# Kernel tuning notes

Hardware: AMD Instinct MI355X
Metric: run time of the kernel (lower is better)

Reference implementation:

```python
import jax, jax.numpy as jnp
import numpy as np

NUM_EXPERTS = 32
TOP_K = 4
HIDDEN = 2048
INTER = 768
N_TOKENS = 2048
NORM_TOPK = True


def setup_inputs() -> dict:
    key = jax.random.key(0)
    k0, k1, k2, k3 = jax.random.split(key, 4)
    hidden_states = jax.random.normal(k0, (N_TOKENS, HIDDEN), dtype=jnp.float32)
    # router gate: Linear(hidden, num_experts), stored as (h, E)
    Wg = jax.random.normal(k1, (HIDDEN, NUM_EXPERTS), dtype=jnp.float32) * 0.02
    # per-expert merged gate_up: (E, h, 2*i); down: (E, i, h)
    Wgu = jax.random.normal(k2, (NUM_EXPERTS, HIDDEN, 2 * INTER), dtype=jnp.float32) * 0.02
    Wd = jax.random.normal(k3, (NUM_EXPERTS, INTER, HIDDEN), dtype=jnp.float32) * 0.02
    return {"hidden_states": hidden_states, "Wg": Wg, "Wgu": Wgu, "Wd": Wd}


def reference(hidden_states, Wg, Wgu, Wd):
    E = Wgu.shape[0]
    # ---- routing ----
    router_logits = hidden_states @ Wg                       # (N, E)
    probs = jax.nn.softmax(router_logits.astype(jnp.float32), axis=-1)
    topk_w, topk_idx = jax.lax.top_k(probs, TOP_K)           # (N, K)
    if NORM_TOPK:
        topk_w = topk_w / jnp.sum(topk_w, axis=-1, keepdims=True)
    topk_w = topk_w.astype(hidden_states.dtype)
    # dense combine weights: (N, E), zero where expert not selected
    combine = jnp.einsum("nke,nk->ne", jax.nn.one_hot(topk_idx, E, dtype=topk_w.dtype), topk_w)
    # ---- experts (dense dispatch, zero-weighted combine == gather/scatter math) ----
    gate_up = jnp.einsum("nh,ehf->nef", hidden_states, Wgu)  # (N, E, 2i)
    gate, up = jnp.split(gate_up, 2, axis=-1)                # (N, E, i) each
    y = jax.nn.silu(gate) * up                               # SiluAndMul
    y = y * combine[:, :, None]                              # apply routing weight before down-proj (linear -> equivalent)
    out = jnp.einsum("nef,efh->nh", y, Wd)                   # (N, h)
    return out
```

## Files before the change

kernel.cpp:

```cpp
#include <hip/hip_runtime.h>
#include <hip/hip_bf16.h>

#define NE 32
#define TOPK 4
#define HID 2048
#define INTER 768
#define NT 2048
#define MAXTILE 64

typedef float f32x4 __attribute__((ext_vector_type(4)));
typedef float f32x2 __attribute__((ext_vector_type(2)));
typedef unsigned int u32x4 __attribute__((ext_vector_type(4)));
typedef unsigned int u32x2 __attribute__((ext_vector_type(2)));
typedef short short8 __attribute__((ext_vector_type(8)));
typedef __bf16 bf16x8 __attribute__((ext_vector_type(8)));

__device__ inline unsigned short f2bf(float f) {
  unsigned u = __builtin_bit_cast(unsigned, f);
  u += 0x7fffu + ((u >> 16) & 1u);
  return (unsigned short)(u >> 16);
}
__device__ inline unsigned pack2(unsigned short a, unsigned short b) {
  return (unsigned)a | ((unsigned)b << 16);
}
__device__ inline f32x4 mfma_bf16(short8 a, short8 b, f32x4 c) {
  return __builtin_amdgcn_mfma_f32_16x16x32_bf16(
      __builtin_bit_cast(bf16x8, a), __builtin_bit_cast(bf16x8, b), c, 0, 0, 0);
}
__device__ inline void gload16(const void* g, void* l) {
  __builtin_amdgcn_global_load_lds(
      (const __attribute__((address_space(1))) void*)g,
      (__attribute__((address_space(3))) void*)l, 16, 0, 0);
}

__global__ __launch_bounds__(64) void k_router(const float* __restrict__ X,
                                               const float* __restrict__ Wg,
                                               int* __restrict__ expert_of,
                                               float* __restrict__ weight_of,
                                               int* __restrict__ counts) {
  const int n = blockIdx.x;
  const int lane = threadIdx.x;
  const float* x = X + (size_t)n * HID;
  float acc[NE];
#pragma unroll
  for (int e = 0; e < NE; ++e) acc[e] = 0.f;
  for (int h = lane; h < HID; h += 64) {
    const float xv = x[h];
    const f32x4* wr = (const f32x4*)(Wg + (size_t)h * NE);
#pragma unroll
    for (int q = 0; q < NE / 4; ++q) {
      f32x4 w4 = wr[q];
      acc[q * 4 + 0] += xv * w4[0];
      acc[q * 4 + 1] += xv * w4[1];
      acc[q * 4 + 2] += xv * w4[2];
      acc[q * 4 + 3] += xv * w4[3];
    }
  }
#pragma unroll
  for (int off = 32; off >= 1; off >>= 1) {
#pragma unroll
    for (int e = 0; e < NE; ++e) acc[e] += __shfl_xor(acc[e], off, 64);
  }
  if (lane == 0) {
    float m = acc[0];
#pragma unroll
    for (int e = 1; e < NE; ++e) m = fmaxf(m, acc[e]);
    unsigned used = 0;
    int idx[TOPK];
    float wv[TOPK];
    float wsum = 0.f;
    for (int k = 0; k < TOPK; ++k) {
      int best = 0;
      float bv = -1e30f;
      for (int e = 0; e < NE; ++e) {
        if (!((used >> e) & 1u) && acc[e] > bv) { bv = acc[e]; best = e; }
      }
      used |= 1u << best;
      float w = expf(bv - m);
      idx[k] = best;
      wv[k] = w;
      wsum += w;
    }
    const float inv = 1.f / wsum;
    for (int k = 0; k < TOPK; ++k) {
      expert_of[n * TOPK + k] = idx[k];
      weight_of[n * TOPK + k] = wv[k] * inv;
      atomicAdd(&counts[idx[k]], 1);
    }
  }
}

__global__ void k_scan(const int* __restrict__ counts, int* __restrict__ offsets,
                       int* __restrict__ wl_e, int* __restrict__ wl_m,
                       int* __restrict__ wl_n) {
  int s = 0, t = 0;
  for (int e = 0; e < NE; ++e) {
    offsets[e] = s;
    const int c = counts[e];
    for (int m0 = 0; m0 < c; m0 += 256) {
      wl_e[t] = e;
      wl_m[t] = m0;
      ++t;
    }
    s += c;
  }
  offsets[NE] = s;
  *wl_n = t;
}

__global__ __launch_bounds__(64) void k_scatter(const int* __restrict__ expert_of,
                                                const float* __restrict__ weight_of,
                                                const int* __restrict__ offsets,
                                                int* __restrict__ slot_token,
                                                float* __restrict__ slot_w) {
  const int e = blockIdx.x;
  const int lane = threadIdx.x;
  int cnt = offsets[e];
  for (int a0 = 0; a0 < NT * TOPK; a0 += 64) {
    const int a = a0 + lane;
    const bool m = (expert_of[a] == e);
    const unsigned long long bal = __ballot(m);
    if (m) {
      const int pos = cnt + __popcll(bal & ((1ull << lane) - 1ull));
      slot_token[pos] = a >> 2;
      slot_w[pos] = weight_of[a];
    }
    cnt += __popcll(bal);
  }
}

__global__ __launch_bounds__(256) void k_xconv(const float* __restrict__ X,
                                               unsigned short* __restrict__ Xb) {
  const int i = blockIdx.x * 256 + threadIdx.x;
  const f32x4 v = ((const f32x4*)X)[i];
  u32x2 t = {pack2(f2bf(v[0]), f2bf(v[1])), pack2(f2bf(v[2]), f2bf(v[3]))};
  ((u32x2*)Xb)[i] = t;
}

__global__ __launch_bounds__(512) void k_gemm1(const unsigned short* __restrict__ Xb,
                                               const float* __restrict__ Wgu,
                                               const int* __restrict__ slot_token,
                                               const float* __restrict__ slot_w,
                                               const int* __restrict__ offsets,
                                               const int* __restrict__ wl_e,
                                               const int* __restrict__ wl_m,
                                               const int* __restrict__ wl_n,
                                               unsigned short* __restrict__ Y) {
  const int tile = blockIdx.x;
  if (tile >= *wl_n) return;
  const int e = wl_e[tile];
  const int m0 = wl_m[tile];
  const int base = offsets[e];
  const int ne = offsets[e + 1] - base;
  const int n0 = blockIdx.y * 64;
  const int tid = threadIdx.x;
  const int lane = tid & 63, w = tid >> 6;
  const int wm = w >> 1, wn = w & 1;
  const int fr = lane & 15, fo = lane >> 4;
  const int lr = lane >> 3, lk = lane & 7;

  __shared__ __attribute__((aligned(16))) unsigned short As[256 * 64];
  __shared__ __attribute__((aligned(16))) unsigned short Bg[64 * 64];
  __shared__ __attribute__((aligned(16))) unsigned short Bu[64 * 64];

  f32x4 accg[4][2], accu[4][2];
#pragma unroll
  for (int i = 0; i < 4; ++i)
#pragma unroll
    for (int j = 0; j < 2; ++j) {
      f32x4 z = {0.f, 0.f, 0.f, 0.f};
      accg[i][j] = z;
      accu[i][j] = z;
    }

  const unsigned short* asrc[4];
#pragma unroll
  for (int i = 0; i < 4; ++i) {
    const int ra = (w * 4 + i) * 8 + lr;
    const int tok = slot_token[base + min(m0 + ra, ne - 1)];
    asrc[i] = Xb + (size_t)tok * HID + ((lk ^ (ra & 7)) << 3);
  }

  const int np = tid & 31, kg = (tid >> 5) & 7, rg = tid >> 8;
  const float* bsrc = Wgu + (size_t)e * HID * (2 * INTER) + (size_t)(kg * 8) * (2 * INTER) +
                      rg * INTER + n0 + 2 * np;
  unsigned short* Bd = rg ? Bu : Bg;
  const int n_a = 2 * np, n_b = 2 * np + 1;
  const int wofa = n_a * 64 + ((kg ^ (n_a & 7)) << 3);
  const int wofb = n_b * 64 + ((kg ^ (n_b & 7)) << 3);

  for (int k0 = 0; k0 < HID; k0 += 64) {
#pragma unroll
    for (int i = 0; i < 4; ++i) gload16(asrc[i] + k0, &As[(w * 4 + i) * 512]);
    const float* bp = bsrc + (size_t)k0 * (2 * INTER);
    f32x2 bv[8];
#pragma unroll
    for (int j = 0; j < 8; ++j) bv[j] = *(const f32x2*)(bp + (size_t)j * (2 * INTER));
    u32x4 ta = {pack2(f2bf(bv[0][0]), f2bf(bv[1][0])), pack2(f2bf(bv[2][0]), f2bf(bv[3][0])),
                pack2(f2bf(bv[4][0]), f2bf(bv[5][0])), pack2(f2bf(bv[6][0]), f2bf(bv[7][0]))};
    u32x4 tb = {pack2(f2bf(bv[0][1]), f2bf(bv[1][1])), pack2(f2bf(bv[2][1]), f2bf(bv[3][1])),
                pack2(f2bf(bv[4][1]), f2bf(bv[5][1])), pack2(f2bf(bv[6][1]), f2bf(bv[7][1]))};
    *(u32x4*)&Bd[wofa] = ta;
    *(u32x4*)&Bd[wofb] = tb;
    __syncthreads();
#pragma unroll
    for (int ks = 0; ks < 2; ++ks) {
      const int c = ks * 4 + fo;
      short8 a[4], bg[2], bu[2];
#pragma unroll
      for (int mi = 0; mi < 4; ++mi) {
        const int row = wm * 64 + mi * 16 + fr;
        a[mi] = *(const short8*)&As[row * 64 + ((c ^ (row & 7)) << 3)];
      }
#pragma unroll
      for (int ni = 0; ni < 2; ++ni) {
        const int row = wn * 32 + ni * 16 + fr;
        const int off = row * 64 + ((c ^ (row & 7)) << 3);
        bg[ni] = *(const short8*)&Bg[off];
        bu[ni] = *(const short8*)&Bu[off];
      }
#pragma unroll
      for (int mi = 0; mi < 4; ++mi)
#pragma unroll
        for (int ni = 0; ni < 2; ++ni) {
          accg[mi][ni] = mfma_bf16(a[mi], bg[ni], accg[mi][ni]);
          accu[mi][ni] = mfma_bf16(a[mi], bu[ni], accu[mi][ni]);
        }
    }
    __syncthreads();
  }

#pragma unroll
  for (int mi = 0; mi < 4; ++mi) {
#pragma unroll
    for (int j = 0; j < 4; ++j) {
      const int gm = m0 + wm * 64 + mi * 16 + fo * 4 + j;
      if (gm < ne) {
        const float wgt = slot_w[base + gm];
        unsigned short* yp = Y + (size_t)(base + gm) * INTER + n0 + wn * 32;
#pragma unroll
        for (int ni = 0; ni < 2; ++ni) {
          const float g = accg[mi][ni][j];
          const float u = accu[mi][ni][j];
          const float yv = (g / (1.0f + __expf(-g))) * u * wgt;
          yp[ni * 16 + fr] = f2bf(yv);
        }
      }
    }
  }
}

__global__ __launch_bounds__(512) void k_gemm2(const unsigned short* __restrict__ Y,
                                               const float* __restrict__ Wd,
                                               const int* __restrict__ slot_token,
                                               const int* __restrict__ offsets,
                                               const int* __restrict__ wl_e,
                                               const int* __restrict__ wl_m,
                                               const int* __restrict__ wl_n,
                                               float* __restrict__ out) {
  const int tile = blockIdx.x;
  if (tile >= *wl_n) return;
  const int e = wl_e[tile];
  const int m0 = wl_m[tile];
  const int base = offsets[e];
  const int ne = offsets[e + 1] - base;
  const int n0 = blockIdx.y * 128;
  const int tid = threadIdx.x;
  const int lane = tid & 63, w = tid >> 6;
  const int wm = w >> 1, wn = w & 1;
  const int fr = lane & 15, fo = lane >> 4;
  const int lr = lane >> 3, lk = lane & 7;

  __shared__ __attribute__((aligned(16))) unsigned short As[256 * 64];
  __shared__ __attribute__((aligned(16))) unsigned short Bs[128 * 64];

  f32x4 acc[4][4];
#pragma unroll
  for (int i = 0; i < 4; ++i)
#pragma unroll
    for (int j = 0; j < 4; ++j) {
      f32x4 z = {0.f, 0.f, 0.f, 0.f};
      acc[i][j] = z;
    }

  const unsigned short* asrc[4];
#pragma unroll
  for (int i = 0; i < 4; ++i) {
    const int ra = (w * 4 + i) * 8 + lr;
    const int grow = base + min(m0 + ra, ne - 1);
    asrc[i] = Y + (size_t)grow * INTER + ((lk ^ (ra & 7)) << 3);
  }

  const int np = tid & 63, kg = tid >> 6;
  const float* bsrc = Wd + (size_t)e * INTER * HID + (size_t)(kg * 8) * HID + n0 + 2 * np;
  const int n_a = 2 * np, n_b = 2 * np + 1;
  const int wofa = n_a * 64 + ((kg ^ (n_a & 7)) << 3);
  const int wofb = n_b * 64 + ((kg ^ (n_b & 7)) << 3);

  for (int k0 = 0; k0 < INTER; k0 += 64) {
#pragma unroll
    for (int i = 0; i < 4; ++i) gload16(asrc[i] + k0, &As[(w * 4 + i) * 512]);
    const float* bp = bsrc + (size_t)k0 * HID;
    f32x2 bv[8];
#pragma unroll
    for (int j = 0; j < 8; ++j) bv[j] = *(const f32x2*)(bp + (size_t)j * HID);
    u32x4 ta = {pack2(f2bf(bv[0][0]), f2bf(bv[1][0])), pack2(f2bf(bv[2][0]), f2bf(bv[3][0])),
                pack2(f2bf(bv[4][0]), f2bf(bv[5][0])), pack2(f2bf(bv[6][0]), f2bf(bv[7][0]))};
    u32x4 tb = {pack2(f2bf(bv[0][1]), f2bf(bv[1][1])), pack2(f2bf(bv[2][1]), f2bf(bv[3][1])),
                pack2(f2bf(bv[4][1]), f2bf(bv[5][1])), pack2(f2bf(bv[6][1]), f2bf(bv[7][1]))};
    *(u32x4*)&Bs[wofa] = ta;
    *(u32x4*)&Bs[wofb] = tb;
    __syncthreads();
#pragma unroll
    for (int ks = 0; ks < 2; ++ks) {
      const int c = ks * 4 + fo;
      short8 a[4], b[4];
#pragma unroll
      for (int mi = 0; mi < 4; ++mi) {
        const int row = wm * 64 + mi * 16 + fr;
        a[mi] = *(const short8*)&As[row * 64 + ((c ^ (row & 7)) << 3)];
      }
#pragma unroll
      for (int ni = 0; ni < 4; ++ni) {
        const int row = wn * 64 + ni * 16 + fr;
        b[ni] = *(const short8*)&Bs[row * 64 + ((c ^ (row & 7)) << 3)];
      }
#pragma unroll
      for (int mi = 0; mi < 4; ++mi)
#pragma unroll
        for (int ni = 0; ni < 4; ++ni) acc[mi][ni] = mfma_bf16(a[mi], b[ni], acc[mi][ni]);
    }
    __syncthreads();
  }

#pragma unroll
  for (int mi = 0; mi < 4; ++mi) {
#pragma unroll
    for (int j = 0; j < 4; ++j) {
      const int gm = m0 + wm * 64 + mi * 16 + fo * 4 + j;
      if (gm < ne) {
        const int tok = slot_token[base + gm];
        float* op = out + (size_t)tok * HID + n0 + wn * 64;
#pragma unroll
        for (int ni = 0; ni < 4; ++ni) atomicAdd(&op[ni * 16 + fr], acc[mi][ni][j]);
      }
    }
  }
}

extern "C" void kernel_launch(void* const* d_in, const int* in_sizes, int n_in,
                              void* d_out, int out_size, void* d_ws, size_t ws_size,
                              hipStream_t stream) {
  (void)in_sizes; (void)n_in; (void)ws_size;
  const float* X = (const float*)d_in[0];
  const float* Wg = (const float*)d_in[1];
  const float* Wgu = (const float*)d_in[2];
  const float* Wd = (const float*)d_in[3];
  float* out = (float*)d_out;

  char* ws = (char*)d_ws;
  int* counts = (int*)(ws + 0);
  int* offsets = (int*)(ws + 256);
  int* wl_n = (int*)(ws + 512);
  int* wl_e = (int*)(ws + 1024);
  int* wl_m = (int*)(ws + 1536);
  int* expert_of = (int*)(ws + 2048);
  float* weight_of = (float*)(ws + 2048 + 32768);
  int* slot_token = (int*)(ws + 2048 + 2 * 32768);
  float* slot_w = (float*)(ws + 2048 + 3 * 32768);
  unsigned short* Xb = (unsigned short*)(ws + 133120);
  unsigned short* Yb = (unsigned short*)(ws + 8521728);

  hipMemsetAsync(counts, 0, 128, stream);
  hipMemsetAsync(d_out, 0, (size_t)out_size * sizeof(float), stream);

  k_router<<<NT, 64, 0, stream>>>(X, Wg, expert_of, weight_of, counts);
  k_scan<<<1, 1, 0, stream>>>(counts, offsets, wl_e, wl_m, wl_n);
  k_scatter<<<NE, 64, 0, stream>>>(expert_of, weight_of, offsets, slot_token, slot_w);
  k_xconv<<<(NT * HID / 4) / 256, 256, 0, stream>>>(X, Xb);
  k_gemm1<<<dim3(MAXTILE, INTER / 64), 512, 0, stream>>>(Xb, Wgu, slot_token, slot_w,
                                                         offsets, wl_e, wl_m, wl_n, Yb);
  k_gemm2<<<dim3(MAXTILE, HID / 128), 512, 0, stream>>>(Yb, Wd, slot_token, offsets,
                                                        wl_e, wl_m, wl_n, out);
}
```

Baseline: 481.8 us.

## Double-buffer GEMM tiles, fuse bf16 conversion into router, drop scan kernel

```diff
diff --git a/kernel.cpp b/kernel.cpp
--- a/kernel.cpp
+++ b/kernel.cpp
@@ -32,12 +32,30 @@
       (const __attribute__((address_space(1))) void*)g,
       (__attribute__((address_space(3))) void*)l, 16, 0, 0);
 }
+__device__ inline bool locate(const int* __restrict__ counts, int tile, int& e,
+                              int& m0, int& base, int& ne) {
+  int tl = tile;
+  base = 0;
+  for (e = 0; e < NE; ++e) {
+    const int c = counts[e];
+    const int nt = (c + 255) >> 8;
+    if (tl < nt) {
+      m0 = tl << 8;
+      ne = c;
+      return true;
+    }
+    tl -= nt;
+    base += c;
+  }
+  return false;
+}
 
 __global__ __launch_bounds__(64) void k_router(const float* __restrict__ X,
                                                const float* __restrict__ Wg,
                                                int* __restrict__ expert_of,
                                                float* __restrict__ weight_of,
-                                               int* __restrict__ counts) {
+                                               int* __restrict__ counts,
+                                               unsigned short* __restrict__ Xb) {
   const int n = blockIdx.x;
   const int lane = threadIdx.x;
   const float* x = X + (size_t)n * HID;
@@ -55,6 +73,15 @@
       acc[q * 4 + 2] += xv * w4[2];
       acc[q * 4 + 3] += xv * w4[3];
     }
+  }
+  const f32x4* x4 = (const f32x4*)x;
+  u32x2* xb2 = (u32x2*)(Xb + (size_t)n * HID);
+#pragma unroll
+  for (int it = 0; it < HID / 4 / 64; ++it) {
+    const int q = it * 64 + lane;
+    f32x4 v = x4[q];
+    u32x2 t = {pack2(f2bf(v[0]), f2bf(v[1])), pack2(f2bf(v[2]), f2bf(v[3]))};
+    xb2[q] = t;
   }
 #pragma unroll
   for (int off = 32; off >= 1; off >>= 1) {
@@ -90,32 +117,15 @@
   }
 }
 
-__global__ void k_scan(const int* __restrict__ counts, int* __restrict__ offsets,
-                       int* __restrict__ wl_e, int* __restrict__ wl_m,
-                       int* __restrict__ wl_n) {
-  int s = 0, t = 0;
-  for (int e = 0; e < NE; ++e) {
-    offsets[e] = s;
-    const int c = counts[e];
-    for (int m0 = 0; m0 < c; m0 += 256) {
-      wl_e[t] = e;
-      wl_m[t] = m0;
-      ++t;
-    }
-    s += c;
-  }
-  offsets[NE] = s;
-  *wl_n = t;
-}
-
 __global__ __launch_bounds__(64) void k_scatter(const int* __restrict__ expert_of,
                                                 const float* __restrict__ weight_of,
-                                                const int* __restrict__ offsets,
+                                                const int* __restrict__ counts,
                                                 int* __restrict__ slot_token,
                                                 float* __restrict__ slot_w) {
   const int e = blockIdx.x;
   const int lane = threadIdx.x;
-  int cnt = offsets[e];
+  int cnt = 0;
+  for (int i = 0; i < NE; ++i) cnt += (i < e) ? counts[i] : 0;
   for (int a0 = 0; a0 < NT * TOPK; a0 += 64) {
     const int a = a0 + lane;
     const bool m = (expert_of[a] == e);
@@ -129,29 +139,14 @@
   }
 }
 
-__global__ __launch_bounds__(256) void k_xconv(const float* __restrict__ X,
-                                               unsigned short* __restrict__ Xb) {
-  const int i = blockIdx.x * 256 + threadIdx.x;
-  const f32x4 v = ((const f32x4*)X)[i];
-  u32x2 t = {pack2(f2bf(v[0]), f2bf(v[1])), pack2(f2bf(v[2]), f2bf(v[3]))};
-  ((u32x2*)Xb)[i] = t;
-}
-
 __global__ __launch_bounds__(512) void k_gemm1(const unsigned short* __restrict__ Xb,
                                                const float* __restrict__ Wgu,
                                                const int* __restrict__ slot_token,
                                                const float* __restrict__ slot_w,
-                                               const int* __restrict__ offsets,
-                                               const int* __restrict__ wl_e,
-                                               const int* __restrict__ wl_m,
-                                               const int* __restrict__ wl_n,
+                                               const int* __restrict__ counts,
                                                unsigned short* __restrict__ Y) {
-  const int tile = blockIdx.x;
-  if (tile >= *wl_n) return;
-  const int e = wl_e[tile];
-  const int m0 = wl_m[tile];
-  const int base = offsets[e];
-  const int ne = offsets[e + 1] - base;
+  int e, m0, base, ne;
+  if (!locate(counts, blockIdx.x, e, m0, base, ne)) return;
   const int n0 = blockIdx.y * 64;
   const int tid = threadIdx.x;
   const int lane = tid & 63, w = tid >> 6;
@@ -159,9 +154,9 @@
   const int fr = lane & 15, fo = lane >> 4;
   const int lr = lane >> 3, lk = lane & 7;
 
-  __shared__ __attribute__((aligned(16))) unsigned short As[256 * 64];
-  __shared__ __attribute__((aligned(16))) unsigned short Bg[64 * 64];
-  __shared__ __attribute__((aligned(16))) unsigned short Bu[64 * 64];
+  __shared__ __attribute__((aligned(16))) unsigned short As[2][256 * 64];
+  __shared__ __attribute__((aligned(16))) unsigned short Bg[2][64 * 64];
+  __shared__ __attribute__((aligned(16))) unsigned short Bu[2][64 * 64];
 
   f32x4 accg[4][2], accu[4][2];
 #pragma unroll
@@ -182,27 +177,31 @@
   }
 
   const int np = tid & 31, kg = (tid >> 5) & 7, rg = tid >> 8;
-  const float* bsrc = Wgu + (size_t)e * HID * (2 * INTER) + (size_t)(kg * 8) * (2 * INTER) +
-                      rg * INTER + n0 + 2 * np;
-  unsigned short* Bd = rg ? Bu : Bg;
+  const float* bsrc = Wgu + (size_t)e * HID * (2 * INTER) +
+                      (size_t)(kg * 8) * (2 * INTER) + rg * INTER + n0 + 2 * np;
   const int n_a = 2 * np, n_b = 2 * np + 1;
   const int wofa = n_a * 64 + ((kg ^ (n_a & 7)) << 3);
   const int wofb = n_b * 64 + ((kg ^ (n_b & 7)) << 3);
 
-  for (int k0 = 0; k0 < HID; k0 += 64) {
-#pragma unroll
-    for (int i = 0; i < 4; ++i) gload16(asrc[i] + k0, &As[(w * 4 + i) * 512]);
-    const float* bp = bsrc + (size_t)k0 * (2 * INTER);
-    f32x2 bv[8];
+  auto stage_a = [&](int t, int b) {
+#pragma unroll
+    for (int i = 0; i < 4; ++i) gload16(asrc[i] + t * 64, &As[b][(w * 4 + i) * 512]);
+  };
+  auto load_b = [&](int t, f32x2* bv) {
+    const float* bp = bsrc + (size_t)(t * 64) * (2 * INTER);
 #pragma unroll
     for (int j = 0; j < 8; ++j) bv[j] = *(const f32x2*)(bp + (size_t)j * (2 * INTER));
+  };
+  auto pack_write = [&](const f32x2* bv, int b) {
     u32x4 ta = {pack2(f2bf(bv[0][0]), f2bf(bv[1][0])), pack2(f2bf(bv[2][0]), f2bf(bv[3][0])),
                 pack2(f2bf(bv[4][0]), f2bf(bv[5][0])), pack2(f2bf(bv[6][0]), f2bf(bv[7][0]))};
     u32x4 tb = {pack2(f2bf(bv[0][1]), f2bf(bv[1][1])), pack2(f2bf(bv[2][1]), f2bf(bv[3][1])),
                 pack2(f2bf(bv[4][1]), f2bf(bv[5][1])), pack2(f2bf(bv[6][1]), f2bf(bv[7][1]))};
+    unsigned short* Bd = rg ? Bu[b] : Bg[b];
     *(u32x4*)&Bd[wofa] = ta;
     *(u32x4*)&Bd[wofb] = tb;
-    __syncthreads();
+  };
+  auto do_mfma = [&](int b) {
 #pragma unroll
     for (int ks = 0; ks < 2; ++ks) {
       const int c = ks * 4 + fo;
@@ -210,14 +209,14 @@
 #pragma unroll
       for (int mi = 0; mi < 4; ++mi) {
         const int row = wm * 64 + mi * 16 + fr;
-        a[mi] = *(const short8*)&As[row * 64 + ((c ^ (row & 7)) << 3)];
+        a[mi] = *(const short8*)&As[b][row * 64 + ((c ^ (row & 7)) << 3)];
       }
 #pragma unroll
       for (int ni = 0; ni < 2; ++ni) {
         const int row = wn * 32 + ni * 16 + fr;
         const int off = row * 64 + ((c ^ (row & 7)) << 3);
-        bg[ni] = *(const short8*)&Bg[off];
-        bu[ni] = *(const short8*)&Bu[off];
+        bg[ni] = *(const short8*)&Bg[b][off];
+        bu[ni] = *(const short8*)&Bu[b][off];
       }
 #pragma unroll
       for (int mi = 0; mi < 4; ++mi)
@@ -227,6 +226,28 @@
           accu[mi][ni] = mfma_bf16(a[mi], bu[ni], accu[mi][ni]);
         }
     }
+  };
+
+  const int NS = HID / 64;
+  {
+    f32x2 bv[8];
+    stage_a(0, 0);
+    load_b(0, bv);
+    pack_write(bv, 0);
+  }
+  __syncthreads();
+#pragma unroll 2
+  for (int t = 0; t < NS; ++t) {
+    const int cur = t & 1, nxt = cur ^ 1;
+    f32x2 bv[8];
+    const bool more = (t + 1 < NS);
+    if (more) {
+      stage_a(t + 1, nxt);
+      load_b(t + 1, bv);
+    }
+    __builtin_amdgcn_sched_barrier(0);
+    do_mfma(cur);
+    if (more) pack_write(bv, nxt);
     __syncthreads();
   }
 
@@ -253,17 +274,10 @@
 __global__ __launch_bounds__(512) void k_gemm2(const unsigned short* __restrict__ Y,
                                                const float* __restrict__ Wd,
                                                const int* __restrict__ slot_token,
-                                               const int* __restrict__ offsets,
-                                               const int* __restrict__ wl_e,
-                                               const int* __restrict__ wl_m,
-                                               const int* __restrict__ wl_n,
+                                               const int* __restrict__ counts,
                                                float* __restrict__ out) {
-  const int tile = blockIdx.x;
-  if (tile >= *wl_n) return;
-  const int e = wl_e[tile];
-  const int m0 = wl_m[tile];
-  const int base = offsets[e];
-  const int ne = offsets[e + 1] - base;
+  int e, m0, base, ne;
+  if (!locate(counts, blockIdx.x, e, m0, base, ne)) return;
   const int n0 = blockIdx.y * 128;
   const int tid = threadIdx.x;
   const int lane = tid & 63, w = tid >> 6;
@@ -271,8 +285,8 @@
   const int fr = lane & 15, fo = lane >> 4;
   const int lr = lane >> 3, lk = lane & 7;
 
-  __shared__ __attribute__((aligned(16))) unsigned short As[256 * 64];
-  __shared__ __attribute__((aligned(16))) unsigned short Bs[128 * 64];
+  __shared__ __attribute__((aligned(16))) unsigned short As[2][256 * 64];
+  __shared__ __attribute__((aligned(16))) unsigned short Bs[2][128 * 64];
 
   f32x4 acc[4][4];
 #pragma unroll
@@ -297,39 +311,65 @@
   const int wofa = n_a * 64 + ((kg ^ (n_a & 7)) << 3);
   const int wofb = n_b * 64 + ((kg ^ (n_b & 7)) << 3);
 
-  for (int k0 = 0; k0 < INTER; k0 += 64) {
-#pragma unroll
-    for (int i = 0; i < 4; ++i) gload16(asrc[i] + k0, &As[(w * 4 + i) * 512]);
-    const float* bp = bsrc + (size_t)k0 * HID;
-    f32x2 bv[8];
+  auto stage_a = [&](int t, int b) {
+#pragma unroll
+    for (int i = 0; i < 4; ++i) gload16(asrc[i] + t * 64, &As[b][(w * 4 + i) * 512]);
+  };
+  auto load_b = [&](int t, f32x2* bv) {
+    const float* bp = bsrc + (size_t)(t * 64) * HID;
 #pragma unroll
     for (int j = 0; j < 8; ++j) bv[j] = *(const f32x2*)(bp + (size_t)j * HID);
+  };
+  auto pack_write = [&](const f32x2* bv, int b) {
     u32x4 ta = {pack2(f2bf(bv[0][0]), f2bf(bv[1][0])), pack2(f2bf(bv[2][0]), f2bf(bv[3][0])),
                 pack2(f2bf(bv[4][0]), f2bf(bv[5][0])), pack2(f2bf(bv[6][0]), f2bf(bv[7][0]))};
     u32x4 tb = {pack2(f2bf(bv[0][1]), f2bf(bv[1][1])), pack2(f2bf(bv[2][1]), f2bf(bv[3][1])),
                 pack2(f2bf(bv[4][1]), f2bf(bv[5][1])), pack2(f2bf(bv[6][1]), f2bf(bv[7][1]))};
-    *(u32x4*)&Bs[wofa] = ta;
-    *(u32x4*)&Bs[wofb] = tb;
-    __syncthreads();
+    *(u32x4*)&Bs[b][wofa] = ta;
+    *(u32x4*)&Bs[b][wofb] = tb;
+  };
+  auto do_mfma = [&](int b) {
 #pragma unroll
     for (int ks = 0; ks < 2; ++ks) {
       const int c = ks * 4 + fo;
-      short8 a[4], b[4];
+      short8 a[4], bb[4];
 #pragma unroll
       for (int mi = 0; mi < 4; ++mi) {
         const int row = wm * 64 + mi * 16 + fr;
-        a[mi] = *(const short8*)&As[row * 64 + ((c ^ (row & 7)) << 3)];
+        a[mi] = *(const short8*)&As[b][row * 64 + ((c ^ (row & 7)) << 3)];
       }
 #pragma unroll
       for (int ni = 0; ni < 4; ++ni) {
         const int row = wn * 64 + ni * 16 + fr;
-        b[ni] = *(const short8*)&Bs[row * 64 + ((c ^ (row & 7)) << 3)];
+        bb[ni] = *(const short8*)&Bs[b][row * 64 + ((c ^ (row & 7)) << 3)];
       }
 #pragma unroll
       for (int mi = 0; mi < 4; ++mi)
 #pragma unroll
-        for (int ni = 0; ni < 4; ++ni) acc[mi][ni] = mfma_bf16(a[mi], b[ni], acc[mi][ni]);
-    }
+        for (int ni = 0; ni < 4; ++ni) acc[mi][ni] = mfma_bf16(a[mi], bb[ni], acc[mi][ni]);
+    }
+  };
+
+  const int NS = INTER / 64;
+  {
+    f32x2 bv[8];
+    stage_a(0, 0);
+    load_b(0, bv);
+    pack_write(bv, 0);
+  }
+  __syncthreads();
+#pragma unroll 2
+  for (int t = 0; t < NS; ++t) {
+    const int cur = t & 1, nxt = cur ^ 1;
+    f32x2 bv[8];
+    const bool more = (t + 1 < NS);
+    if (more) {
+      stage_a(t + 1, nxt);
+      load_b(t + 1, bv);
+    }
+    __builtin_amdgcn_sched_barrier(0);
+    do_mfma(cur);
+    if (more) pack_write(bv, nxt);
     __syncthreads();
   }
 
@@ -360,10 +400,6 @@
 
   char* ws = (char*)d_ws;
   int* counts = (int*)(ws + 0);
-  int* offsets = (int*)(ws + 256);
-  int* wl_n = (int*)(ws + 512);
-  int* wl_e = (int*)(ws + 1024);
-  int* wl_m = (int*)(ws + 1536);
   int* expert_of = (int*)(ws + 2048);
   float* weight_of = (float*)(ws + 2048 + 32768);
   int* slot_token = (int*)(ws + 2048 + 2 * 32768);
@@ -374,12 +410,9 @@
   hipMemsetAsync(counts, 0, 128, stream);
   hipMemsetAsync(d_out, 0, (size_t)out_size * sizeof(float), stream);
 
-  k_router<<<NT, 64, 0, stream>>>(X, Wg, expert_of, weight_of, counts);
-  k_scan<<<1, 1, 0, stream>>>(counts, offsets, wl_e, wl_m, wl_n);
-  k_scatter<<<NE, 64, 0, stream>>>(expert_of, weight_of, offsets, slot_token, slot_w);
-  k_xconv<<<(NT * HID / 4) / 256, 256, 0, stream>>>(X, Xb);
+  k_router<<<NT, 64, 0, stream>>>(X, Wg, expert_of, weight_of, counts, Xb);
+  k_scatter<<<NE, 64, 0, stream>>>(expert_of, weight_of, counts, slot_token, slot_w);
   k_gemm1<<<dim3(MAXTILE, INTER / 64), 512, 0, stream>>>(Xb, Wgu, slot_token, slot_w,
-                                                         offsets, wl_e, wl_m, wl_n, Yb);
-  k_gemm2<<<dim3(MAXTILE, HID / 128), 512, 0, stream>>>(Yb, Wd, slot_token, offsets,
-                                                        wl_e, wl_m, wl_n, out);
-}
+                                                         counts, Yb);
+  k_gemm2<<<dim3(MAXTILE, HID / 128), 512, 0, stream>>>(Yb, Wd, slot_token, counts, out);
+}
```

Measured after the change: 536.6 us. +11.4%, slower.
